# Kernel tuning notes

Hardware: AMD Instinct MI355X
Metric: run time of the kernel (lower is better)

Reference implementation:

```python
import jax, jax.numpy as jnp
import numpy as np

B, R, NM, H, P1, G1, RC1, LAT = 16384, 360, 200, 256, 512, 256, 256, 128


def _linear_params(k, out_f, in_f):
    s = 1.0 / np.sqrt(in_f)
    kw, kb = jax.random.split(k)
    W = jax.random.uniform(kw, (out_f, in_f), minval=-s, maxval=s, dtype=jnp.float32)
    b = jax.random.uniform(kb, (out_f,), minval=-s, maxval=s, dtype=jnp.float32)
    return W, b


def setup_inputs() -> dict:
    key = jax.random.key(0)
    ks = jax.random.split(key, 14)
    x_window = jax.random.normal(ks[0], (B, 3, R), dtype=jnp.float32)
    modes = jax.random.normal(ks[1], (R, NM), dtype=jnp.float32)
    mode_coeff = jax.random.normal(ks[2], (B, NM), dtype=jnp.float32)
    W1, b1 = _linear_params(ks[3], H, 3 * R)      # surrogate layer 1
    W2, b2 = _linear_params(ks[4], H, H)          # surrogate layer 2
    W3, b3 = _linear_params(ks[5], R, H)          # surrogate layer 3
    Wp1, bp1 = _linear_params(ks[6], P1, R * R)   # npi_proj
    Wp2, bp2 = _linear_params(ks[7], LAT, P1)
    Wg1, bg1 = _linear_params(ks[8], G1, NM)      # geo_proj
    Wg2, bg2 = _linear_params(ks[9], LAT, G1)
    Wr1, br1 = _linear_params(ks[10], RC1, LAT)   # recon
    Wr2, br2 = _linear_params(ks[11], R, RC1)
    return dict(x_window=x_window, modes=modes, mode_coeff=mode_coeff,
                W1=W1, b1=b1, W2=W2, b2=b2, W3=W3, b3=b3,
                Wp1=Wp1, bp1=bp1, Wp2=Wp2, bp2=bp2,
                Wg1=Wg1, bg1=bg1, Wg2=Wg2, bg2=bg2,
                Wr1=Wr1, br1=br1, Wr2=Wr2, br2=br2)


def reference(x_window, modes, mode_coeff,
              W1, b1, W2, b2, W3, b3,
              Wp1, bp1, Wp2, bp2,
              Wg1, bg1, Wg2, bg2,
              Wr1, br1, Wr2, br2):
    Bs = x_window.shape[0]
    Rr = W3.shape[0]
    # ---- NPI surrogate forward (needed for ReLU masks) ----
    z = x_window.reshape(Bs, 3 * Rr)                       # (B, 3R)
    h1 = z @ W1.T + b1                                     # (B, H)
    m1 = (h1 > 0).astype(z.dtype)
    h2 = (h1 * m1) @ W2.T + b2                             # (B, H)
    m2 = (h2 > 0).astype(z.dtype)
    # ---- EC: exact batch-mean Jacobian of the ReLU MLP w.r.t last timestep ----
    # mean_b [ W3 diag(m2_b) W2 diag(m1_b) W1_last ] = W3 @ (W2 * (m2^T m1 / B)) @ W1[:, -R:]
    G = (m2.T @ m1) / Bs                                   # (H, H)
    ec = W3 @ ((W2 * G) @ W1[:, -Rr:])                     # (R, R); row j = dy_j/dx
    ec = jax.lax.stop_gradient(ec)                         # create_graph=False in original
    # ---- projections ----
    ec_flat = ec.reshape(1, Rr * Rr)
    z_npi1 = jax.nn.relu(ec_flat @ Wp1.T + bp1) @ Wp2.T + bp2   # (1, LAT)
    z_npi = jnp.tile(z_npi1, (Bs, 1))                           # (B, LAT)
    z_geo = jax.nn.relu(mode_coeff @ Wg1.T + bg1) @ Wg2.T + bg2  # (B, LAT)
    zsum = z_npi + z_geo
    zn = zsum / jnp.maximum(jnp.linalg.norm(zsum, axis=-1, keepdims=True), 1e-12)
    recon = jax.nn.relu(zn @ Wr1.T + br1) @ Wr2.T + br2          # (B, R)
    return (z_npi, z_geo, zn, ec, recon)
```

## Files before the change

### kernel.cpp

```cpp
#include <hip/hip_runtime.h>

typedef __bf16 bf16x8 __attribute__((ext_vector_type(8)));
typedef __bf16 bf16x4 __attribute__((ext_vector_type(4)));
typedef float  f32x4  __attribute__((ext_vector_type(4)));

__device__ __forceinline__ f32x4 mfma_bf16(bf16x8 a, bf16x8 b, f32x4 c) {
  return __builtin_amdgcn_mfma_f32_16x16x32_bf16(a, b, c, 0, 0, 0);
}
__device__ __forceinline__ bf16x8 ldB(const __bf16* Bp, int kt, int NT, int nt,
                                      int lane) {
  return *reinterpret_cast<const bf16x8*>(Bp + (((size_t)kt * NT + nt) * 64 + lane) * 8);
}

__global__ void pack_all(const float* __restrict__ W1, const float* __restrict__ W2,
                         const float* __restrict__ Wg1, const float* __restrict__ Wg2,
                         const float* __restrict__ Wr1, const float* __restrict__ Wr2,
                         __bf16* __restrict__ W1p, __bf16* __restrict__ W2p,
                         __bf16* __restrict__ Wg1p, __bf16* __restrict__ Wg2p,
                         __bf16* __restrict__ Wr1p, __bf16* __restrict__ Wr2p,
                         float* __restrict__ G) {
  int bx = blockIdx.x;
  int lane = threadIdx.x;
  if (bx >= 1104) {
    float4* g = (float4*)G;
    int base = (bx - 1104) * 512 + lane;
#pragma unroll
    for (int i = 0; i < 8; ++i) g[base + i * 64] = make_float4(0.f, 0.f, 0.f, 0.f);
    return;
  }
  const float* W; __bf16* out; int N, K, NT, local;
  if (bx < 544)      { W = W1;  out = W1p;  N = 256; K = 1080; NT = 16; local = bx; }
  else if (bx < 672) { W = W2;  out = W2p;  N = 256; K = 256;  NT = 16; local = bx - 544; }
  else if (bx < 784) { W = Wg1; out = Wg1p; N = 256; K = 200;  NT = 16; local = bx - 672; }
  else if (bx < 848) { W = Wg2; out = Wg2p; N = 128; K = 256;  NT = 8;  local = bx - 784; }
  else if (bx < 912) { W = Wr1; out = Wr1p; N = 256; K = 128;  NT = 16; local = bx - 848; }
  else               { W = Wr2; out = Wr2p; N = 360; K = 256;  NT = 24; local = bx - 912; }
  int nt = local % NT, kt = local / NT;
  int n = nt * 16 + (lane & 15);
  int k0 = kt * 32 + (lane >> 4) * 8;
  bf16x8 v;
#pragma unroll
  for (int e = 0; e < 8; ++e) {
    int k = k0 + e;
    float xv = (n < N && k < K) ? W[(size_t)n * K + k] : 0.f;
    v[e] = (__bf16)xv;
  }
  *reinterpret_cast<bf16x8*>(out + ((size_t)local * 64 + lane) * 8) = v;
}

__global__ __launch_bounds__(256) void h1h2_fused(
    const float* __restrict__ x, const __bf16* __restrict__ W1p,
    const float* __restrict__ b1, const __bf16* __restrict__ W2p,
    const float* __restrict__ b2, __bf16* __restrict__ m1T,
    __bf16* __restrict__ m2T) {
  __shared__ __bf16 Alds[32][68];
  __shared__ __bf16 h1s[32][264];
  int tid = threadIdx.x;
  int lane = tid & 63, wid = tid >> 6;
  int rowBase = blockIdx.x * 32;
  int sr = tid >> 3, sc = (tid & 7) * 8;
  const float* aSrc = x + (size_t)(rowBase + sr) * 1080;
  f32x4 acc[2][4] = {};
  float4 c0a, c0b, c1a, c1b;
  auto LD = [&](int s, float4& a, float4& b) {
    int gk = s * 64 + sc;
    if (gk < 1080) {
      a = *(const float4*)(aSrc + gk);
      b = *(const float4*)(aSrc + gk + 4);
    } else {
      a = make_float4(0.f, 0.f, 0.f, 0.f);
      b = a;
    }
  };
  LD(0, c0a, c0b);
  LD(1, c1a, c1b);
  for (int s = 0; s < 17; ++s) {
    bf16x8 w8;
    w8[0] = (__bf16)c0a.x; w8[1] = (__bf16)c0a.y; w8[2] = (__bf16)c0a.z; w8[3] = (__bf16)c0a.w;
    w8[4] = (__bf16)c0b.x; w8[5] = (__bf16)c0b.y; w8[6] = (__bf16)c0b.z; w8[7] = (__bf16)c0b.w;
    *reinterpret_cast<bf16x8*>(&Alds[sr][sc]) = w8;
    __syncthreads();
    c0a = c1a; c0b = c1b;
    if (s + 2 < 17) LD(s + 2, c1a, c1b);
    int arow = lane & 15;
#pragma unroll
    for (int ks = 0; ks < 2; ++ks) {
      int ak = ks * 32 + (lane >> 4) * 8;
      bf16x8 a0 = *reinterpret_cast<const bf16x8*>(&Alds[arow][ak]);
      bf16x8 a1 = *reinterpret_cast<const bf16x8*>(&Alds[arow + 16][ak]);
      int kt = s * 2 + ks;
#pragma unroll
      for (int n = 0; n < 4; ++n) {
        bf16x8 bv = ldB(W1p, kt, 16, wid * 4 + n, lane);
        acc[0][n] = mfma_bf16(a0, bv, acc[0][n]);
        acc[1][n] = mfma_bf16(a1, bv, acc[1][n]);
      }
    }
    __syncthreads();
  }
  int q4 = (lane >> 4) * 4;
#pragma unroll
  for (int m = 0; m < 2; ++m)
#pragma unroll
    for (int n = 0; n < 4; ++n) {
      int col = wid * 64 + n * 16 + (lane & 15);
      float bb = b1[col];
#pragma unroll
      for (int j = 0; j < 4; ++j) {
        int rl = m * 16 + q4 + j;
        float h = acc[m][n][j] + bb;
        m1T[(size_t)col * 16384 + rowBase + rl] = (__bf16)(h > 0.f ? 1.f : 0.f);
        h1s[rl][col] = (__bf16)fmaxf(h, 0.f);
      }
    }
  __syncthreads();
  f32x4 acc2[2][4] = {};
#pragma unroll
  for (int ks = 0; ks < 8; ++ks) {
    int arow = lane & 15, ak = ks * 32 + (lane >> 4) * 8;
    bf16x8 a0 = *reinterpret_cast<const bf16x8*>(&h1s[arow][ak]);
    bf16x8 a1 = *reinterpret_cast<const bf16x8*>(&h1s[arow + 16][ak]);
#pragma unroll
    for (int n = 0; n < 4; ++n) {
      bf16x8 bv = ldB(W2p, ks, 16, wid * 4 + n, lane);
      acc2[0][n] = mfma_bf16(a0, bv, acc2[0][n]);
      acc2[1][n] = mfma_bf16(a1, bv, acc2[1][n]);
    }
  }
#pragma unroll
  for (int m = 0; m < 2; ++m)
#pragma unroll
    for (int n = 0; n < 4; ++n) {
      int col = wid * 64 + n * 16 + (lane & 15);
      float bb = b2[col];
#pragma unroll
      for (int j = 0; j < 4; ++j) {
        int rl = m * 16 + q4 + j;
        float h = acc2[m][n][j] + bb;
        m2T[(size_t)col * 16384 + rowBase + rl] = (__bf16)(h > 0.f ? 1.f : 0.f);
      }
    }
}

__global__ __launch_bounds__(256) void gemm_masks(
    const __bf16* __restrict__ m2T, const __bf16* __restrict__ m1T,
    float* __restrict__ G) {
  int tid = threadIdx.x;
  int lane = tid & 63, wid = tid >> 6;
  int wr = wid >> 1, wc = wid & 1;
  int ibase = blockIdx.x * 64, jbase = blockIdx.y * 64;
  size_t b0 = (size_t)blockIdx.z * 1024 + (lane >> 4) * 8;
  const __bf16* pa0 = m2T + (size_t)(ibase + wr * 32 + (lane & 15)) * 16384 + b0;
  const __bf16* pa1 = pa0 + (size_t)16 * 16384;
  const __bf16* pb0 = m1T + (size_t)(jbase + wc * 32 + (lane & 15)) * 16384 + b0;
  const __bf16* pb1 = pb0 + (size_t)16 * 16384;
  f32x4 acc[2][2] = {};
#pragma unroll 4
  for (int c = 0; c < 32; ++c) {
    bf16x8 a0 = *reinterpret_cast<const bf16x8*>(pa0 + c * 32);
    bf16x8 a1 = *reinterpret_cast<const bf16x8*>(pa1 + c * 32);
    bf16x8 bv0 = *reinterpret_cast<const bf16x8*>(pb0 + c * 32);
    bf16x8 bv1 = *reinterpret_cast<const bf16x8*>(pb1 + c * 32);
    acc[0][0] = mfma_bf16(a0, bv0, acc[0][0]);
    acc[0][1] = mfma_bf16(a0, bv1, acc[0][1]);
    acc[1][0] = mfma_bf16(a1, bv0, acc[1][0]);
    acc[1][1] = mfma_bf16(a1, bv1, acc[1][1]);
  }
  int q4 = (lane >> 4) * 4;
#pragma unroll
  for (int m = 0; m < 2; ++m)
#pragma unroll
    for (int n = 0; n < 2; ++n)
#pragma unroll
      for (int j = 0; j < 4; ++j) {
        int gi = ibase + wr * 32 + m * 16 + q4 + j;
        int gj = jbase + wc * 32 + n * 16 + (lane & 15);
        atomicAdd(&G[(size_t)gi * 256 + gj], acc[m][n][j] * (1.f / 16384.f));
      }
}

__global__ __launch_bounds__(256) void small_gemm(
    const float* __restrict__ A, const float* __restrict__ A2, int lda,
    const float* __restrict__ Bm, int ldb, float* __restrict__ C, int ldc,
    int M, int N, int K) {
  __shared__ float As[64][17];
  __shared__ float Bs[16][65];
  int t = threadIdx.x;
  int tx = t & 15, ty = t >> 4;
  int m0 = blockIdx.y * 64, n0 = blockIdx.x * 64;
  float acc[4][4] = {};
  for (int k0 = 0; k0 < K; k0 += 16) {
#pragma unroll
    for (int i = 0; i < 4; ++i) {
      int idx = t * 4 + i;
      int r = idx >> 4, kk = idx & 15;
      int gm = m0 + r, gk = k0 + kk;
      float v = (gm < M && gk < K) ? A[(size_t)gm * lda + gk] : 0.f;
      if (A2 && gm < M && gk < K) v *= A2[(size_t)gm * lda + gk];
      As[r][kk] = v;
      int kk2 = idx >> 6, cc = idx & 63;
      int gk2 = k0 + kk2, gn = n0 + cc;
      Bs[kk2][cc] = (gk2 < K && gn < N) ? Bm[(size_t)gk2 * ldb + gn] : 0.f;
    }
    __syncthreads();
#pragma unroll
    for (int kk = 0; kk < 16; ++kk)
#pragma unroll
      for (int i = 0; i < 4; ++i)
#pragma unroll
        for (int j = 0; j < 4; ++j)
          acc[i][j] += As[ty * 4 + i][kk] * Bs[kk][tx * 4 + j];
    __syncthreads();
  }
#pragma unroll
  for (int i = 0; i < 4; ++i)
#pragma unroll
    for (int j = 0; j < 4; ++j) {
      int gm = m0 + ty * 4 + i, gn = n0 + tx * 4 + j;
      if (gm < M && gn < N) C[(size_t)gm * ldc + gn] = acc[i][j];
    }
}

__global__ __launch_bounds__(512) void p_and_g1(
    const float* __restrict__ Wp1, const float* __restrict__ ec,
    const float* __restrict__ bp1, float* __restrict__ p,
    const float* __restrict__ mc, const __bf16* __restrict__ Wg1p,
    const float* __restrict__ bg1, const __bf16* __restrict__ Wg2p,
    const float* __restrict__ bg2, float* __restrict__ o_zgeo) {
  __shared__ __bf16 Alds[64][40];
  __shared__ __bf16 g1S[64][264];
  __shared__ float redw[8];
  int t = threadIdx.x;
  if (blockIdx.x < 512) {
    int row = blockIdx.x;
    const float4* w = (const float4*)(Wp1 + (size_t)row * 129600);
    const float4* e = (const float4*)ec;
    float s = 0.f;
    for (int i = t; i < 32400; i += 512) {
      float4 a = w[i], b = e[i];
      s += a.x * b.x + a.y * b.y + a.z * b.z + a.w * b.w;
    }
    for (int o = 32; o; o >>= 1) s += __shfl_down(s, o);
    if ((t & 63) == 0) redw[t >> 6] = s;
    __syncthreads();
    if (t == 0) {
      float tot = 0.f;
#pragma unroll
      for (int i = 0; i < 8; ++i) tot += redw[i];
      p[row] = fmaxf(tot + bp1[row], 0.f);
    }
  } else {
    int lane = t & 63, wid = t >> 6;
    int wr = wid >> 2, wc = wid & 3;
    int rowBase = (blockIdx.x - 512) * 64;
    int sr = t >> 3, sc = (t & 7) * 4;
    const float* aSrc = mc + (size_t)(rowBase + sr) * 200;
    int q4 = (lane >> 4) * 4;
    f32x4 acc[2][4] = {};
    for (int kt = 0; kt < 7; ++kt) {
      int gk = kt * 32 + sc;
      bf16x4 w4;
      if (gk < 200) {
        float4 v = *(const float4*)(aSrc + gk);
        w4[0] = (__bf16)v.x; w4[1] = (__bf16)v.y;
        w4[2] = (__bf16)v.z; w4[3] = (__bf16)v.w;
      } else {
        w4[0] = w4[1] = w4[2] = w4[3] = (__bf16)0.f;
      }
      *reinterpret_cast<bf16x4*>(&Alds[sr][sc]) = w4;
      __syncthreads();
      int arow = wr * 32 + (lane & 15), ak = (lane >> 4) * 8;
      bf16x8 a0 = *reinterpret_cast<const bf16x8*>(&Alds[arow][ak]);
      bf16x8 a1 = *reinterpret_cast<const bf16x8*>(&Alds[arow + 16][ak]);
#pragma unroll
      for (int n = 0; n < 4; ++n) {
        bf16x8 bv = ldB(Wg1p, kt, 16, wc * 4 + n, lane);
        acc[0][n] = mfma_bf16(a0, bv, acc[0][n]);
        acc[1][n] = mfma_bf16(a1, bv, acc[1][n]);
      }
      __syncthreads();
    }
#pragma unroll
    for (int m = 0; m < 2; ++m)
#pragma unroll
      for (int n = 0; n < 4; ++n) {
        int col = wc * 64 + n * 16 + (lane & 15);
        float bb = bg1[col];
#pragma unroll
        for (int j = 0; j < 4; ++j) {
          int rl = wr * 32 + m * 16 + q4 + j;
          g1S[rl][col] = (__bf16)fmaxf(acc[m][n][j] + bb, 0.f);
        }
      }
    __syncthreads();
    f32x4 acc2[2][2] = {};
#pragma unroll
    for (int ks = 0; ks < 8; ++ks) {
      int arow = wr * 32 + (lane & 15), ak = ks * 32 + (lane >> 4) * 8;
      bf16x8 a0 = *reinterpret_cast<const bf16x8*>(&g1S[arow][ak]);
      bf16x8 a1 = *reinterpret_cast<const bf16x8*>(&g1S[arow + 16][ak]);
#pragma unroll
      for (int n = 0; n < 2; ++n) {
        bf16x8 bv = ldB(Wg2p, ks, 8, wc * 2 + n, lane);
        acc2[0][n] = mfma_bf16(a0, bv, acc2[0][n]);
        acc2[1][n] = mfma_bf16(a1, bv, acc2[1][n]);
      }
    }
#pragma unroll
    for (int m = 0; m < 2; ++m)
#pragma unroll
      for (int n = 0; n < 2; ++n) {
        int col = wc * 32 + n * 16 + (lane & 15);
        float bb = bg2[col];
#pragma unroll
        for (int j = 0; j < 4; ++j) {
          int row = rowBase + wr * 32 + m * 16 + q4 + j;
          o_zgeo[(size_t)row * 128 + col] = acc2[m][n][j] + bb;
        }
      }
  }
}

__global__ void gemv_z(const float* __restrict__ p, const float* __restrict__ Wp2,
                       const float* __restrict__ bp2, float* __restrict__ znpi1) {
  int j = blockIdx.x;
  int t = threadIdx.x;
  const float4* w = (const float4*)(Wp2 + (size_t)j * 512);
  const float4* pp = (const float4*)p;
  float4 a0 = w[t], b0 = pp[t];
  float4 a1 = w[t + 64], b1 = pp[t + 64];
  float s = a0.x * b0.x + a0.y * b0.y + a0.z * b0.z + a0.w * b0.w +
            a1.x * b1.x + a1.y * b1.y + a1.z * b1.z + a1.w * b1.w;
  for (int o = 32; o; o >>= 1) s += __shfl_down(s, o);
  if (t == 0) znpi1[j] = s + bp2[j];
}

__global__ __launch_bounds__(512) void mega_tail(
    const float* __restrict__ zgeo, const float* __restrict__ znpi1,
    const __bf16* __restrict__ Wr1p, const float* __restrict__ br1,
    const __bf16* __restrict__ Wr2p, const float* __restrict__ br2,
    float* __restrict__ o_znpi, float* __restrict__ o_zn,
    float* __restrict__ o_rec) {
  __shared__ __bf16 r1S[64][264];
  __shared__ __bf16 znS[64][136];
  __shared__ float znpiS[128];
  int tid = threadIdx.x;
  int lane = tid & 63, wid = tid >> 6;
  int wr = wid >> 2, wc = wid & 3;
  int rowBase = blockIdx.x * 64;
  int q4 = (lane >> 4) * 4;
  if (tid < 128) znpiS[tid] = znpi1[tid];
  __syncthreads();
  {
    int rg = tid >> 5;
    int c4 = (tid & 31) * 4;
    float4 zp = make_float4(znpiS[c4], znpiS[c4 + 1], znpiS[c4 + 2], znpiS[c4 + 3]);
#pragma unroll
    for (int ri = 0; ri < 4; ++ri) {
      int rl = rg + ri * 16;
      int row = rowBase + rl;
      float4 zg = *(const float4*)(zgeo + (size_t)row * 128 + c4);
      float4 zs = make_float4(zg.x + zp.x, zg.y + zp.y, zg.z + zp.z, zg.w + zp.w);
      *(float4*)(o_znpi + (size_t)row * 128 + c4) = zp;
      float ss = zs.x * zs.x + zs.y * zs.y + zs.z * zs.z + zs.w * zs.w;
      ss += __shfl_xor(ss, 1);
      ss += __shfl_xor(ss, 2);
      ss += __shfl_xor(ss, 4);
      ss += __shfl_xor(ss, 8);
      ss += __shfl_xor(ss, 16);
      float rn = 1.f / fmaxf(sqrtf(ss), 1e-12f);
      float4 zn = make_float4(zs.x * rn, zs.y * rn, zs.z * rn, zs.w * rn);
      *(float4*)(o_zn + (size_t)row * 128 + c4) = zn;
      bf16x4 znb;
      znb[0] = (__bf16)zn.x; znb[1] = (__bf16)zn.y;
      znb[2] = (__bf16)zn.z; znb[3] = (__bf16)zn.w;
      *reinterpret_cast<bf16x4*>(&znS[rl][c4]) = znb;
    }
  }
  __syncthreads();
  {
    f32x4 acc[2][4] = {};
#pragma unroll
    for (int ks = 0; ks < 4; ++ks) {
      int arow = wr * 32 + (lane & 15), ak = ks * 32 + (lane >> 4) * 8;
      bf16x8 a0 = *reinterpret_cast<const bf16x8*>(&znS[arow][ak]);
      bf16x8 a1 = *reinterpret_cast<const bf16x8*>(&znS[arow + 16][ak]);
#pragma unroll
      for (int n = 0; n < 4; ++n) {
        bf16x8 bv = ldB(Wr1p, ks, 16, wc * 4 + n, lane);
        acc[0][n] = mfma_bf16(a0, bv, acc[0][n]);
        acc[1][n] = mfma_bf16(a1, bv, acc[1][n]);
      }
    }
#pragma unroll
    for (int m = 0; m < 2; ++m)
#pragma unroll
      for (int n = 0; n < 4; ++n) {
        int col = wc * 64 + n * 16 + (lane & 15);
        float bb = br1[col];
#pragma unroll
        for (int j = 0; j < 4; ++j) {
          int rl = wr * 32 + m * 16 + q4 + j;
          r1S[rl][col] = (__bf16)fmaxf(acc[m][n][j] + bb, 0.f);
        }
      }
  }
  __syncthreads();
  {
    f32x4 acc[2][6] = {};
#pragma unroll
    for (int ks = 0; ks < 8; ++ks) {
      int arow = wr * 32 + (lane & 15), ak = ks * 32 + (lane >> 4) * 8;
      bf16x8 a0 = *reinterpret_cast<const bf16x8*>(&r1S[arow][ak]);
      bf16x8 a1 = *reinterpret_cast<const bf16x8*>(&r1S[arow + 16][ak]);
#pragma unroll
      for (int n = 0; n < 6; ++n) {
        bf16x8 bv = ldB(Wr2p, ks, 24, wc * 6 + n, lane);
        acc[0][n] = mfma_bf16(a0, bv, acc[0][n]);
        acc[1][n] = mfma_bf16(a1, bv, acc[1][n]);
      }
    }
#pragma unroll
    for (int m = 0; m < 2; ++m)
#pragma unroll
      for (int n = 0; n < 6; ++n) {
        int col = wc * 96 + n * 16 + (lane & 15);
        if (col < 360) {
          float bb = br2[col];
#pragma unroll
          for (int j = 0; j < 4; ++j) {
            int rl = wr * 32 + m * 16 + q4 + j;
            o_rec[(size_t)(rowBase + rl) * 360 + col] = acc[m][n][j] + bb;
          }
        }
      }
  }
}

extern "C" void kernel_launch(void* const* d_in, const int* in_sizes, int n_in,
                              void* d_out, int out_size, void* d_ws,
                              size_t ws_size, hipStream_t stream) {
  (void)in_sizes; (void)n_in; (void)out_size; (void)ws_size;
  const float* x   = (const float*)d_in[0];
  const float* mc  = (const float*)d_in[2];
  const float* W1  = (const float*)d_in[3];  const float* b1  = (const float*)d_in[4];
  const float* W2  = (const float*)d_in[5];  const float* b2  = (const float*)d_in[6];
  const float* W3  = (const float*)d_in[7];
  const float* Wp1 = (const float*)d_in[9];  const float* bp1 = (const float*)d_in[10];
  const float* Wp2 = (const float*)d_in[11]; const float* bp2 = (const float*)d_in[12];
  const float* Wg1 = (const float*)d_in[13]; const float* bg1 = (const float*)d_in[14];
  const float* Wg2 = (const float*)d_in[15]; const float* bg2 = (const float*)d_in[16];
  const float* Wr1 = (const float*)d_in[17]; const float* br1 = (const float*)d_in[18];
  const float* Wr2 = (const float*)d_in[19]; const float* br2 = (const float*)d_in[20];

  float* out = (float*)d_out;
  float* o_znpi = out;
  float* o_zgeo = out + 2097152;
  float* o_zn   = out + 4194304;
  float* o_ec   = out + 6291456;
  float* o_rec  = out + 6421056;

  char* ws = (char*)d_ws;
  __bf16* m1T   = (__bf16*)(ws + 0);
  __bf16* m2T   = (__bf16*)(ws + 8388608);
  float*  G     = (float*)(ws + 16777216);
  float*  T     = (float*)(ws + 17039360);
  float*  p512  = (float*)(ws + 17432576);
  float*  znpi1 = (float*)(ws + 17434624);
  __bf16* W1p   = (__bf16*)(ws + 17435648);
  __bf16* W2p   = W1p  + (size_t)544 * 512;
  __bf16* Wg1p  = W2p  + (size_t)128 * 512;
  __bf16* Wg2p  = Wg1p + (size_t)112 * 512;
  __bf16* Wr1p  = Wg2p + (size_t)64 * 512;
  __bf16* Wr2p  = Wr1p + (size_t)64 * 512;

  pack_all<<<1136, 64, 0, stream>>>(W1, W2, Wg1, Wg2, Wr1, Wr2,
                                    W1p, W2p, Wg1p, Wg2p, Wr1p, Wr2p, G);
  h1h2_fused<<<512, 256, 0, stream>>>(x, W1p, b1, W2p, b2, m1T, m2T);
  gemm_masks<<<dim3(4, 4, 16), 256, 0, stream>>>(m2T, m1T, G);
  small_gemm<<<dim3(6, 4), 256, 0, stream>>>(W2, G, 256, W1 + 720, 1080, T, 384,
                                             256, 360, 256);
  small_gemm<<<dim3(6, 6), 256, 0, stream>>>(W3, nullptr, 256, T, 384, o_ec, 360,
                                             360, 360, 256);
  p_and_g1<<<768, 512, 0, stream>>>(Wp1, o_ec, bp1, p512, mc, Wg1p, bg1,
                                    Wg2p, bg2, o_zgeo);
  gemv_z<<<128, 64, 0, stream>>>(p512, Wp2, bp2, znpi1);
  mega_tail<<<256, 512, 0, stream>>>(o_zgeo, znpi1, Wr1p, br1, Wr2p, br2,
                                     o_znpi, o_zn, o_rec);
}
```

Measured before the change: 245.9 us.

## Merge pipeline into two persistent kernels synchronized by software grid barriers

Replaces the eight separate launches (pack, h1/h2, mask gemm, two small gemms, projection, gemv, tail) with two persistent 512-block kernels that use atomic-counter grid barriers between phases. Work is redistributed per block: 32-row tiles with 8 waves, the mask gemm split-K is changed to 32 chunks with wider tiles, and the z_npi gemv is folded into the tail. This is meant to remove launch overhead and inter-kernel gaps. In exchange it relies on all 512 blocks being co-resident for the spin barriers, adds a memset, and idles blocks during the small gemm phases.

```diff
diff --git a/kernel.cpp b/kernel.cpp
--- a/kernel.cpp
+++ b/kernel.cpp
@@ -12,250 +12,229 @@
   return *reinterpret_cast<const bf16x8*>(Bp + (((size_t)kt * NT + nt) * 64 + lane) * 8);
 }
 
-__global__ void pack_all(const float* __restrict__ W1, const float* __restrict__ W2,
-                         const float* __restrict__ Wg1, const float* __restrict__ Wg2,
-                         const float* __restrict__ Wr1, const float* __restrict__ Wr2,
-                         __bf16* __restrict__ W1p, __bf16* __restrict__ W2p,
-                         __bf16* __restrict__ Wg1p, __bf16* __restrict__ Wg2p,
-                         __bf16* __restrict__ Wr1p, __bf16* __restrict__ Wr2p,
-                         float* __restrict__ G) {
-  int bx = blockIdx.x;
-  int lane = threadIdx.x;
-  if (bx >= 1104) {
-    float4* g = (float4*)G;
-    int base = (bx - 1104) * 512 + lane;
-#pragma unroll
-    for (int i = 0; i < 8; ++i) g[base + i * 64] = make_float4(0.f, 0.f, 0.f, 0.f);
-    return;
-  }
-  const float* W; __bf16* out; int N, K, NT, local;
-  if (bx < 544)      { W = W1;  out = W1p;  N = 256; K = 1080; NT = 16; local = bx; }
-  else if (bx < 672) { W = W2;  out = W2p;  N = 256; K = 256;  NT = 16; local = bx - 544; }
-  else if (bx < 784) { W = Wg1; out = Wg1p; N = 256; K = 200;  NT = 16; local = bx - 672; }
-  else if (bx < 848) { W = Wg2; out = Wg2p; N = 128; K = 256;  NT = 8;  local = bx - 784; }
-  else if (bx < 912) { W = Wr1; out = Wr1p; N = 256; K = 128;  NT = 16; local = bx - 848; }
-  else               { W = Wr2; out = Wr2p; N = 360; K = 256;  NT = 24; local = bx - 912; }
-  int nt = local % NT, kt = local / NT;
-  int n = nt * 16 + (lane & 15);
-  int k0 = kt * 32 + (lane >> 4) * 8;
-  bf16x8 v;
-#pragma unroll
-  for (int e = 0; e < 8; ++e) {
-    int k = k0 + e;
-    float xv = (n < N && k < K) ? W[(size_t)n * K + k] : 0.f;
-    v[e] = (__bf16)xv;
-  }
-  *reinterpret_cast<bf16x8*>(out + ((size_t)local * 64 + lane) * 8) = v;
-}
-
-__global__ __launch_bounds__(256) void h1h2_fused(
-    const float* __restrict__ x, const __bf16* __restrict__ W1p,
-    const float* __restrict__ b1, const __bf16* __restrict__ W2p,
-    const float* __restrict__ b2, __bf16* __restrict__ m1T,
-    __bf16* __restrict__ m2T) {
-  __shared__ __bf16 Alds[32][68];
-  __shared__ __bf16 h1s[32][264];
-  int tid = threadIdx.x;
+__device__ __forceinline__ void gridbar(int* cnt, int target) {
+  __syncthreads();
+  if (threadIdx.x == 0) {
+    __threadfence();
+    __hip_atomic_fetch_add(cnt, 1, __ATOMIC_RELEASE, __HIP_MEMORY_SCOPE_AGENT);
+    while (__hip_atomic_load(cnt, __ATOMIC_RELAXED, __HIP_MEMORY_SCOPE_AGENT) < target)
+      __builtin_amdgcn_s_sleep(4);
+    __threadfence();
+  }
+  __syncthreads();
+}
+
+__device__ void small_body(char* SM, int t,
+                           const float* __restrict__ A, const float* __restrict__ A2,
+                           int lda, const float* __restrict__ Bm, int ldb,
+                           float* __restrict__ C, int ldc,
+                           int M, int N, int K, int m0, int n0) {
+  float (*As)[17] = (float(*)[17])SM;
+  float (*Bs)[65] = (float(*)[65])(SM + 4352);
+  bool act = t < 256;
+  int tx = t & 15, ty = (t >> 4) & 15;
+  float acc[4][4] = {};
+  for (int k0 = 0; k0 < K; k0 += 16) {
+    if (act) {
+#pragma unroll
+      for (int i = 0; i < 4; ++i) {
+        int idx = t * 4 + i;
+        int r = idx >> 4, kk = idx & 15;
+        int gm = m0 + r, gk = k0 + kk;
+        float v = (gm < M && gk < K) ? A[(size_t)gm * lda + gk] : 0.f;
+        if (A2 && gm < M && gk < K) v *= A2[(size_t)gm * lda + gk];
+        As[r][kk] = v;
+        int kk2 = idx >> 6, cc = idx & 63;
+        int gk2 = k0 + kk2, gn = n0 + cc;
+        Bs[kk2][cc] = (gk2 < K && gn < N) ? Bm[(size_t)gk2 * ldb + gn] : 0.f;
+      }
+    }
+    __syncthreads();
+    if (act) {
+#pragma unroll
+      for (int kk = 0; kk < 16; ++kk)
+#pragma unroll
+        for (int i = 0; i < 4; ++i)
+#pragma unroll
+          for (int j = 0; j < 4; ++j)
+            acc[i][j] += As[ty * 4 + i][kk] * Bs[kk][tx * 4 + j];
+    }
+    __syncthreads();
+  }
+  if (act) {
+#pragma unroll
+    for (int i = 0; i < 4; ++i)
+#pragma unroll
+      for (int j = 0; j < 4; ++j) {
+        int gm = m0 + ty * 4 + i, gn = n0 + tx * 4 + j;
+        if (gm < M && gn < N) C[(size_t)gm * ldc + gn] = acc[i][j];
+      }
+  }
+}
+
+__global__ __launch_bounds__(512, 4) void mega1(
+    const float* __restrict__ x,
+    const float* __restrict__ W1, const float* __restrict__ b1,
+    const float* __restrict__ W2, const float* __restrict__ b2,
+    const float* __restrict__ W3, const float* __restrict__ mc,
+    const float* __restrict__ Wg1, const float* __restrict__ bg1,
+    const float* __restrict__ Wg2, const float* __restrict__ bg2,
+    const float* __restrict__ Wr1, const float* __restrict__ Wr2,
+    __bf16* __restrict__ W1p, __bf16* __restrict__ W2p,
+    __bf16* __restrict__ Wg1p, __bf16* __restrict__ Wg2p,
+    __bf16* __restrict__ Wr1p, __bf16* __restrict__ Wr2p,
+    __bf16* __restrict__ m1T, __bf16* __restrict__ m2T,
+    float* __restrict__ G, float* __restrict__ T,
+    float* __restrict__ o_zgeo, float* __restrict__ o_ec,
+    int* __restrict__ cnt) {
+  __shared__ __align__(16) char SM[38912];
+  int tid = threadIdx.x, bid = blockIdx.x;
   int lane = tid & 63, wid = tid >> 6;
-  int rowBase = blockIdx.x * 32;
-  int sr = tid >> 3, sc = (tid & 7) * 8;
-  const float* aSrc = x + (size_t)(rowBase + sr) * 1080;
-  f32x4 acc[2][4] = {};
-  float4 c0a, c0b, c1a, c1b;
-  auto LD = [&](int s, float4& a, float4& b) {
-    int gk = s * 64 + sc;
-    if (gk < 1080) {
-      a = *(const float4*)(aSrc + gk);
-      b = *(const float4*)(aSrc + gk + 4);
-    } else {
-      a = make_float4(0.f, 0.f, 0.f, 0.f);
-      b = a;
-    }
-  };
-  LD(0, c0a, c0b);
-  LD(1, c1a, c1b);
-  for (int s = 0; s < 17; ++s) {
-    bf16x8 w8;
-    w8[0] = (__bf16)c0a.x; w8[1] = (__bf16)c0a.y; w8[2] = (__bf16)c0a.z; w8[3] = (__bf16)c0a.w;
-    w8[4] = (__bf16)c0b.x; w8[5] = (__bf16)c0b.y; w8[6] = (__bf16)c0b.z; w8[7] = (__bf16)c0b.w;
-    *reinterpret_cast<bf16x8*>(&Alds[sr][sc]) = w8;
-    __syncthreads();
-    c0a = c1a; c0b = c1b;
-    if (s + 2 < 17) LD(s + 2, c1a, c1b);
-    int arow = lane & 15;
-#pragma unroll
-    for (int ks = 0; ks < 2; ++ks) {
-      int ak = ks * 32 + (lane >> 4) * 8;
-      bf16x8 a0 = *reinterpret_cast<const bf16x8*>(&Alds[arow][ak]);
-      bf16x8 a1 = *reinterpret_cast<const bf16x8*>(&Alds[arow + 16][ak]);
-      int kt = s * 2 + ks;
-#pragma unroll
-      for (int n = 0; n < 4; ++n) {
-        bf16x8 bv = ldB(W1p, kt, 16, wid * 4 + n, lane);
-        acc[0][n] = mfma_bf16(a0, bv, acc[0][n]);
-        acc[1][n] = mfma_bf16(a1, bv, acc[1][n]);
-      }
-    }
-    __syncthreads();
-  }
   int q4 = (lane >> 4) * 4;
-#pragma unroll
-  for (int m = 0; m < 2; ++m)
+
+  {
+    int gid = bid * 8 + wid;
+    if (gid < 1104) {
+      const float* W; __bf16* outp; int N, K, NT, local;
+      if (gid < 544)      { W = W1;  outp = W1p;  N = 256; K = 1080; NT = 16; local = gid; }
+      else if (gid < 672) { W = W2;  outp = W2p;  N = 256; K = 256;  NT = 16; local = gid - 544; }
+      else if (gid < 784) { W = Wg1; outp = Wg1p; N = 256; K = 200;  NT = 16; local = gid - 672; }
+      else if (gid < 848) { W = Wg2; outp = Wg2p; N = 128; K = 256;  NT = 8;  local = gid - 784; }
+      else if (gid < 912) { W = Wr1; outp = Wr1p; N = 256; K = 128;  NT = 16; local = gid - 848; }
+      else                { W = Wr2; outp = Wr2p; N = 360; K = 256;  NT = 24; local = gid - 912; }
+      int nt = local % NT, kt = local / NT;
+      int n = nt * 16 + (lane & 15);
+      int k0 = kt * 32 + (lane >> 4) * 8;
+      bf16x8 v;
+#pragma unroll
+      for (int e = 0; e < 8; ++e) {
+        int k = k0 + e;
+        float xv = (n < N && k < K) ? W[(size_t)n * K + k] : 0.f;
+        v[e] = (__bf16)xv;
+      }
+      *reinterpret_cast<bf16x8*>(outp + ((size_t)local * 64 + lane) * 8) = v;
+    } else if (gid < 1136) {
+      float4* g = (float4*)G;
+      int base = (gid - 1104) * 512 + lane;
+#pragma unroll
+      for (int i = 0; i < 8; ++i) g[base + i * 64] = make_float4(0.f, 0.f, 0.f, 0.f);
+    }
+  }
+  gridbar(cnt, 512);
+
+  {
+    __bf16 (*Alds)[68] = (__bf16(*)[68])SM;
+    __bf16 (*h1s)[264] = (__bf16(*)[264])(SM + 4352);
+    int wr16 = (wid >> 2) * 16, wc4 = (wid & 3) * 4, wc64 = (wid & 3) * 64;
+    int rowBase = bid * 32;
+    int sr = tid >> 4, sc = (tid & 15) * 4;
+    const float* aSrc = x + (size_t)(rowBase + sr) * 1080;
+    f32x4 acc[4] = {};
+    float4 c0, c1;
+    auto LD = [&](int s, float4& d) {
+      int gk = s * 64 + sc;
+      d = (gk < 1080) ? *(const float4*)(aSrc + gk) : make_float4(0.f, 0.f, 0.f, 0.f);
+    };
+    LD(0, c0);
+    LD(1, c1);
+    for (int s = 0; s < 17; ++s) {
+      bf16x4 w4;
+      w4[0] = (__bf16)c0.x; w4[1] = (__bf16)c0.y;
+      w4[2] = (__bf16)c0.z; w4[3] = (__bf16)c0.w;
+      *reinterpret_cast<bf16x4*>(&Alds[sr][sc]) = w4;
+      __syncthreads();
+      c0 = c1;
+      if (s + 2 < 17) LD(s + 2, c1);
+      int arow = wr16 + (lane & 15);
+#pragma unroll
+      for (int ks = 0; ks < 2; ++ks) {
+        int ak = ks * 32 + (lane >> 4) * 8;
+        bf16x8 a0 = *reinterpret_cast<const bf16x8*>(&Alds[arow][ak]);
+        int kt = s * 2 + ks;
+#pragma unroll
+        for (int n = 0; n < 4; ++n) {
+          bf16x8 bv = ldB(W1p, kt, 16, wc4 + n, lane);
+          acc[n] = mfma_bf16(a0, bv, acc[n]);
+        }
+      }
+      __syncthreads();
+    }
 #pragma unroll
     for (int n = 0; n < 4; ++n) {
-      int col = wid * 64 + n * 16 + (lane & 15);
+      int col = wc64 + n * 16 + (lane & 15);
       float bb = b1[col];
 #pragma unroll
       for (int j = 0; j < 4; ++j) {
-        int rl = m * 16 + q4 + j;
-        float h = acc[m][n][j] + bb;
+        int rl = wr16 + q4 + j;
+        float h = acc[n][j] + bb;
         m1T[(size_t)col * 16384 + rowBase + rl] = (__bf16)(h > 0.f ? 1.f : 0.f);
         h1s[rl][col] = (__bf16)fmaxf(h, 0.f);
       }
     }
-  __syncthreads();
-  f32x4 acc2[2][4] = {};
-#pragma unroll
-  for (int ks = 0; ks < 8; ++ks) {
-    int arow = lane & 15, ak = ks * 32 + (lane >> 4) * 8;
-    bf16x8 a0 = *reinterpret_cast<const bf16x8*>(&h1s[arow][ak]);
-    bf16x8 a1 = *reinterpret_cast<const bf16x8*>(&h1s[arow + 16][ak]);
+    __syncthreads();
+    f32x4 acc2[4] = {};
+#pragma unroll
+    for (int ks = 0; ks < 8; ++ks) {
+      int arow = wr16 + (lane & 15), ak = ks * 32 + (lane >> 4) * 8;
+      bf16x8 a0 = *reinterpret_cast<const bf16x8*>(&h1s[arow][ak]);
+#pragma unroll
+      for (int n = 0; n < 4; ++n) {
+        bf16x8 bv = ldB(W2p, ks, 16, wc4 + n, lane);
+        acc2[n] = mfma_bf16(a0, bv, acc2[n]);
+      }
+    }
 #pragma unroll
     for (int n = 0; n < 4; ++n) {
-      bf16x8 bv = ldB(W2p, ks, 16, wid * 4 + n, lane);
-      acc2[0][n] = mfma_bf16(a0, bv, acc2[0][n]);
-      acc2[1][n] = mfma_bf16(a1, bv, acc2[1][n]);
-    }
-  }
-#pragma unroll
-  for (int m = 0; m < 2; ++m)
-#pragma unroll
-    for (int n = 0; n < 4; ++n) {
-      int col = wid * 64 + n * 16 + (lane & 15);
+      int col = wc64 + n * 16 + (lane & 15);
       float bb = b2[col];
 #pragma unroll
       for (int j = 0; j < 4; ++j) {
-        int rl = m * 16 + q4 + j;
-        float h = acc2[m][n][j] + bb;
+        int rl = wr16 + q4 + j;
+        float h = acc2[n][j] + bb;
         m2T[(size_t)col * 16384 + rowBase + rl] = (__bf16)(h > 0.f ? 1.f : 0.f);
       }
     }
-}
-
-__global__ __launch_bounds__(256) void gemm_masks(
-    const __bf16* __restrict__ m2T, const __bf16* __restrict__ m1T,
-    float* __restrict__ G) {
-  int tid = threadIdx.x;
-  int lane = tid & 63, wid = tid >> 6;
-  int wr = wid >> 1, wc = wid & 1;
-  int ibase = blockIdx.x * 64, jbase = blockIdx.y * 64;
-  size_t b0 = (size_t)blockIdx.z * 1024 + (lane >> 4) * 8;
-  const __bf16* pa0 = m2T + (size_t)(ibase + wr * 32 + (lane & 15)) * 16384 + b0;
-  const __bf16* pa1 = pa0 + (size_t)16 * 16384;
-  const __bf16* pb0 = m1T + (size_t)(jbase + wc * 32 + (lane & 15)) * 16384 + b0;
-  const __bf16* pb1 = pb0 + (size_t)16 * 16384;
-  f32x4 acc[2][2] = {};
+  }
+  gridbar(cnt, 1024);
+
+  if (bid < 256) {
+    int iz = bid & 31, ij = bid >> 5;
+    int ibase = (ij >> 1) * 64, jbase = (ij & 1) * 128;
+    int wr = wid >> 2, wc = wid & 3;
+    size_t b0 = (size_t)iz * 512 + (lane >> 4) * 8;
+    const __bf16* pa0 = m2T + (size_t)(ibase + wr * 32 + (lane & 15)) * 16384 + b0;
+    const __bf16* pa1 = pa0 + (size_t)16 * 16384;
+    const __bf16* pb0 = m1T + (size_t)(jbase + wc * 32 + (lane & 15)) * 16384 + b0;
+    const __bf16* pb1 = pb0 + (size_t)16 * 16384;
+    f32x4 acc[2][2] = {};
 #pragma unroll 4
-  for (int c = 0; c < 32; ++c) {
-    bf16x8 a0 = *reinterpret_cast<const bf16x8*>(pa0 + c * 32);
-    bf16x8 a1 = *reinterpret_cast<const bf16x8*>(pa1 + c * 32);
-    bf16x8 bv0 = *reinterpret_cast<const bf16x8*>(pb0 + c * 32);
-    bf16x8 bv1 = *reinterpret_cast<const bf16x8*>(pb1 + c * 32);
-    acc[0][0] = mfma_bf16(a0, bv0, acc[0][0]);
-    acc[0][1] = mfma_bf16(a0, bv1, acc[0][1]);
-    acc[1][0] = mfma_bf16(a1, bv0, acc[1][0]);
-    acc[1][1] = mfma_bf16(a1, bv1, acc[1][1]);
-  }
-  int q4 = (lane >> 4) * 4;
-#pragma unroll
-  for (int m = 0; m < 2; ++m)
-#pragma unroll
-    for (int n = 0; n < 2; ++n)
-#pragma unroll
-      for (int j = 0; j < 4; ++j) {
-        int gi = ibase + wr * 32 + m * 16 + q4 + j;
-        int gj = jbase + wc * 32 + n * 16 + (lane & 15);
-        atomicAdd(&G[(size_t)gi * 256 + gj], acc[m][n][j] * (1.f / 16384.f));
-      }
-}
-
-__global__ __launch_bounds__(256) void small_gemm(
-    const float* __restrict__ A, const float* __restrict__ A2, int lda,
-    const float* __restrict__ Bm, int ldb, float* __restrict__ C, int ldc,
-    int M, int N, int K) {
-  __shared__ float As[64][17];
-  __shared__ float Bs[16][65];
-  int t = threadIdx.x;
-  int tx = t & 15, ty = t >> 4;
-  int m0 = blockIdx.y * 64, n0 = blockIdx.x * 64;
-  float acc[4][4] = {};
-  for (int k0 = 0; k0 < K; k0 += 16) {
-#pragma unroll
-    for (int i = 0; i < 4; ++i) {
-      int idx = t * 4 + i;
-      int r = idx >> 4, kk = idx & 15;
-      int gm = m0 + r, gk = k0 + kk;
-      float v = (gm < M && gk < K) ? A[(size_t)gm * lda + gk] : 0.f;
-      if (A2 && gm < M && gk < K) v *= A2[(size_t)gm * lda + gk];
-      As[r][kk] = v;
-      int kk2 = idx >> 6, cc = idx & 63;
-      int gk2 = k0 + kk2, gn = n0 + cc;
-      Bs[kk2][cc] = (gk2 < K && gn < N) ? Bm[(size_t)gk2 * ldb + gn] : 0.f;
-    }
-    __syncthreads();
-#pragma unroll
-    for (int kk = 0; kk < 16; ++kk)
-#pragma unroll
-      for (int i = 0; i < 4; ++i)
-#pragma unroll
-        for (int j = 0; j < 4; ++j)
-          acc[i][j] += As[ty * 4 + i][kk] * Bs[kk][tx * 4 + j];
-    __syncthreads();
-  }
-#pragma unroll
-  for (int i = 0; i < 4; ++i)
-#pragma unroll
-    for (int j = 0; j < 4; ++j) {
-      int gm = m0 + ty * 4 + i, gn = n0 + tx * 4 + j;
-      if (gm < M && gn < N) C[(size_t)gm * ldc + gn] = acc[i][j];
-    }
-}
-
-__global__ __launch_bounds__(512) void p_and_g1(
-    const float* __restrict__ Wp1, const float* __restrict__ ec,
-    const float* __restrict__ bp1, float* __restrict__ p,
-    const float* __restrict__ mc, const __bf16* __restrict__ Wg1p,
-    const float* __restrict__ bg1, const __bf16* __restrict__ Wg2p,
-    const float* __restrict__ bg2, float* __restrict__ o_zgeo) {
-  __shared__ __bf16 Alds[64][40];
-  __shared__ __bf16 g1S[64][264];
-  __shared__ float redw[8];
-  int t = threadIdx.x;
-  if (blockIdx.x < 512) {
-    int row = blockIdx.x;
-    const float4* w = (const float4*)(Wp1 + (size_t)row * 129600);
-    const float4* e = (const float4*)ec;
-    float s = 0.f;
-    for (int i = t; i < 32400; i += 512) {
-      float4 a = w[i], b = e[i];
-      s += a.x * b.x + a.y * b.y + a.z * b.z + a.w * b.w;
-    }
-    for (int o = 32; o; o >>= 1) s += __shfl_down(s, o);
-    if ((t & 63) == 0) redw[t >> 6] = s;
-    __syncthreads();
-    if (t == 0) {
-      float tot = 0.f;
-#pragma unroll
-      for (int i = 0; i < 8; ++i) tot += redw[i];
-      p[row] = fmaxf(tot + bp1[row], 0.f);
-    }
+    for (int c = 0; c < 16; ++c) {
+      bf16x8 a0 = *reinterpret_cast<const bf16x8*>(pa0 + c * 32);
+      bf16x8 a1 = *reinterpret_cast<const bf16x8*>(pa1 + c * 32);
+      bf16x8 bv0 = *reinterpret_cast<const bf16x8*>(pb0 + c * 32);
+      bf16x8 bv1 = *reinterpret_cast<const bf16x8*>(pb1 + c * 32);
+      acc[0][0] = mfma_bf16(a0, bv0, acc[0][0]);
+      acc[0][1] = mfma_bf16(a0, bv1, acc[0][1]);
+      acc[1][0] = mfma_bf16(a1, bv0, acc[1][0]);
+      acc[1][1] = mfma_bf16(a1, bv1, acc[1][1]);
+    }
+#pragma unroll
+    for (int m = 0; m < 2; ++m)
+#pragma unroll
+      for (int n = 0; n < 2; ++n)
+#pragma unroll
+        for (int j = 0; j < 4; ++j) {
+          int gi = ibase + wr * 32 + m * 16 + q4 + j;
+          int gj = jbase + wc * 32 + n * 16 + (lane & 15);
+          atomicAdd(&G[(size_t)gi * 256 + gj], acc[m][n][j] * (1.f / 16384.f));
+        }
   } else {
-    int lane = t & 63, wid = t >> 6;
+    __bf16 (*Alds2)[40] = (__bf16(*)[40])SM;
+    __bf16 (*g1S)[264] = (__bf16(*)[264])(SM + 5120);
     int wr = wid >> 2, wc = wid & 3;
-    int rowBase = (blockIdx.x - 512) * 64;
-    int sr = t >> 3, sc = (t & 7) * 4;
+    int rowBase = (bid - 256) * 64;
+    int sr = tid >> 3, sc = (tid & 7) * 4;
     const float* aSrc = mc + (size_t)(rowBase + sr) * 200;
-    int q4 = (lane >> 4) * 4;
     f32x4 acc[2][4] = {};
     for (int kt = 0; kt < 7; ++kt) {
       int gk = kt * 32 + sc;
@@ -267,11 +246,11 @@
       } else {
         w4[0] = w4[1] = w4[2] = w4[3] = (__bf16)0.f;
       }
-      *reinterpret_cast<bf16x4*>(&Alds[sr][sc]) = w4;
+      *reinterpret_cast<bf16x4*>(&Alds2[sr][sc]) = w4;
       __syncthreads();
       int arow = wr * 32 + (lane & 15), ak = (lane >> 4) * 8;
-      bf16x8 a0 = *reinterpret_cast<const bf16x8*>(&Alds[arow][ak]);
-      bf16x8 a1 = *reinterpret_cast<const bf16x8*>(&Alds[arow + 16][ak]);
+      bf16x8 a0 = *reinterpret_cast<const bf16x8*>(&Alds2[arow][ak]);
+      bf16x8 a1 = *reinterpret_cast<const bf16x8*>(&Alds2[arow + 16][ak]);
 #pragma unroll
       for (int n = 0; n < 4; ++n) {
         bf16x8 bv = ldB(Wg1p, kt, 16, wc * 4 + n, lane);
@@ -319,109 +298,137 @@
         }
       }
   }
-}
-
-__global__ void gemv_z(const float* __restrict__ p, const float* __restrict__ Wp2,
-                       const float* __restrict__ bp2, float* __restrict__ znpi1) {
-  int j = blockIdx.x;
-  int t = threadIdx.x;
-  const float4* w = (const float4*)(Wp2 + (size_t)j * 512);
-  const float4* pp = (const float4*)p;
-  float4 a0 = w[t], b0 = pp[t];
-  float4 a1 = w[t + 64], b1 = pp[t + 64];
-  float s = a0.x * b0.x + a0.y * b0.y + a0.z * b0.z + a0.w * b0.w +
-            a1.x * b1.x + a1.y * b1.y + a1.z * b1.z + a1.w * b1.w;
-  for (int o = 32; o; o >>= 1) s += __shfl_down(s, o);
-  if (t == 0) znpi1[j] = s + bp2[j];
-}
-
-__global__ __launch_bounds__(512) void mega_tail(
-    const float* __restrict__ zgeo, const float* __restrict__ znpi1,
+  gridbar(cnt, 1536);
+
+  if (bid < 24)
+    small_body(SM, tid, W2, G, 256, W1 + 720, 1080, T, 384,
+               256, 360, 256, (bid / 6) * 64, (bid % 6) * 64);
+  gridbar(cnt, 2048);
+
+  if (bid < 36)
+    small_body(SM, tid, W3, nullptr, 256, T, 384, o_ec, 360,
+               360, 360, 256, (bid / 6) * 64, (bid % 6) * 64);
+}
+
+__global__ __launch_bounds__(512, 4) void mega2(
+    const float* __restrict__ Wp1, const float* __restrict__ ec,
+    const float* __restrict__ bp1, float* __restrict__ p,
+    const float* __restrict__ Wp2, const float* __restrict__ bp2,
+    const float* __restrict__ zgeo,
     const __bf16* __restrict__ Wr1p, const float* __restrict__ br1,
     const __bf16* __restrict__ Wr2p, const float* __restrict__ br2,
     float* __restrict__ o_znpi, float* __restrict__ o_zn,
-    float* __restrict__ o_rec) {
-  __shared__ __bf16 r1S[64][264];
-  __shared__ __bf16 znS[64][136];
-  __shared__ float znpiS[128];
-  int tid = threadIdx.x;
+    float* __restrict__ o_rec, int* __restrict__ cnt) {
+  __shared__ __align__(16) char SM[28160];
+  int tid = threadIdx.x, bid = blockIdx.x;
   int lane = tid & 63, wid = tid >> 6;
-  int wr = wid >> 2, wc = wid & 3;
-  int rowBase = blockIdx.x * 64;
   int q4 = (lane >> 4) * 4;
-  if (tid < 128) znpiS[tid] = znpi1[tid];
-  __syncthreads();
+
   {
-    int rg = tid >> 5;
-    int c4 = (tid & 31) * 4;
-    float4 zp = make_float4(znpiS[c4], znpiS[c4 + 1], znpiS[c4 + 2], znpiS[c4 + 3]);
-#pragma unroll
-    for (int ri = 0; ri < 4; ++ri) {
-      int rl = rg + ri * 16;
-      int row = rowBase + rl;
-      float4 zg = *(const float4*)(zgeo + (size_t)row * 128 + c4);
-      float4 zs = make_float4(zg.x + zp.x, zg.y + zp.y, zg.z + zp.z, zg.w + zp.w);
-      *(float4*)(o_znpi + (size_t)row * 128 + c4) = zp;
-      float ss = zs.x * zs.x + zs.y * zs.y + zs.z * zs.z + zs.w * zs.w;
-      ss += __shfl_xor(ss, 1);
-      ss += __shfl_xor(ss, 2);
-      ss += __shfl_xor(ss, 4);
-      ss += __shfl_xor(ss, 8);
-      ss += __shfl_xor(ss, 16);
-      float rn = 1.f / fmaxf(sqrtf(ss), 1e-12f);
-      float4 zn = make_float4(zs.x * rn, zs.y * rn, zs.z * rn, zs.w * rn);
-      *(float4*)(o_zn + (size_t)row * 128 + c4) = zn;
-      bf16x4 znb;
-      znb[0] = (__bf16)zn.x; znb[1] = (__bf16)zn.y;
-      znb[2] = (__bf16)zn.z; znb[3] = (__bf16)zn.w;
-      *reinterpret_cast<bf16x4*>(&znS[rl][c4]) = znb;
-    }
-  }
-  __syncthreads();
+    float* redw = (float*)SM;
+    const float4* w = (const float4*)(Wp1 + (size_t)bid * 129600);
+    const float4* e = (const float4*)ec;
+    float s = 0.f;
+    for (int i = tid; i < 32400; i += 512) {
+      float4 a = w[i], b = e[i];
+      s += a.x * b.x + a.y * b.y + a.z * b.z + a.w * b.w;
+    }
+    for (int o = 32; o; o >>= 1) s += __shfl_down(s, o);
+    if (lane == 0) redw[wid] = s;
+    __syncthreads();
+    if (tid == 0) {
+      float tot = 0.f;
+#pragma unroll
+      for (int i = 0; i < 8; ++i) tot += redw[i];
+      p[bid] = fmaxf(tot + bp1[bid], 0.f);
+    }
+  }
+  gridbar(cnt, 512);
+
   {
-    f32x4 acc[2][4] = {};
-#pragma unroll
-    for (int ks = 0; ks < 4; ++ks) {
-      int arow = wr * 32 + (lane & 15), ak = ks * 32 + (lane >> 4) * 8;
-      bf16x8 a0 = *reinterpret_cast<const bf16x8*>(&znS[arow][ak]);
-      bf16x8 a1 = *reinterpret_cast<const bf16x8*>(&znS[arow + 16][ak]);
-#pragma unroll
-      for (int n = 0; n < 4; ++n) {
-        bf16x8 bv = ldB(Wr1p, ks, 16, wc * 4 + n, lane);
-        acc[0][n] = mfma_bf16(a0, bv, acc[0][n]);
-        acc[1][n] = mfma_bf16(a1, bv, acc[1][n]);
-      }
-    }
-#pragma unroll
-    for (int m = 0; m < 2; ++m)
+    float* pS = (float*)SM;
+    float* znpiS = (float*)(SM + 2048);
+    __bf16 (*znS)[136] = (__bf16(*)[136])(SM + 2560);
+    __bf16 (*r1S)[264] = (__bf16(*)[264])(SM + 11264);
+    int rowBase = bid * 32;
+    pS[tid] = p[tid];
+    __syncthreads();
+    {
+      int col = tid >> 2, q = tid & 3;
+      const float4* w = (const float4*)(Wp2 + (size_t)col * 512 + q * 128);
+      const float4* pv = (const float4*)(pS + q * 128);
+      float s = 0.f;
+#pragma unroll
+      for (int i = 0; i < 32; ++i) {
+        float4 a = w[i], b = pv[i];
+        s += a.x * b.x + a.y * b.y + a.z * b.z + a.w * b.w;
+      }
+      s += __shfl_xor(s, 1);
+      s += __shfl_xor(s, 2);
+      if (q == 0) znpiS[col] = s + bp2[col];
+    }
+    __syncthreads();
+    {
+      int rg = tid >> 5, c4 = (tid & 31) * 4;
+      float4 zp = make_float4(znpiS[c4], znpiS[c4 + 1], znpiS[c4 + 2], znpiS[c4 + 3]);
+#pragma unroll
+      for (int ri = 0; ri < 2; ++ri) {
+        int rl = rg + ri * 16;
+        int row = rowBase + rl;
+        float4 zg = *(const float4*)(zgeo + (size_t)row * 128 + c4);
+        float4 zs = make_float4(zg.x + zp.x, zg.y + zp.y, zg.z + zp.z, zg.w + zp.w);
+        *(float4*)(o_znpi + (size_t)row * 128 + c4) = zp;
+        float ss = zs.x * zs.x + zs.y * zs.y + zs.z * zs.z + zs.w * zs.w;
+        ss += __shfl_xor(ss, 1);
+        ss += __shfl_xor(ss, 2);
+        ss += __shfl_xor(ss, 4);
+        ss += __shfl_xor(ss, 8);
+        ss += __shfl_xor(ss, 16);
+        float rn = 1.f / fmaxf(sqrtf(ss), 1e-12f);
+        float4 zn = make_float4(zs.x * rn, zs.y * rn, zs.z * rn, zs.w * rn);
+        *(float4*)(o_zn + (size_t)row * 128 + c4) = zn;
+        bf16x4 znb;
+        znb[0] = (__bf16)zn.x; znb[1] = (__bf16)zn.y;
+        znb[2] = (__bf16)zn.z; znb[3] = (__bf16)zn.w;
+        *reinterpret_cast<bf16x4*>(&znS[rl][c4]) = znb;
+      }
+    }
+    __syncthreads();
+    int wr16 = (wid >> 2) * 16, wc = wid & 3;
+    {
+      f32x4 acc[4] = {};
+#pragma unroll
+      for (int ks = 0; ks < 4; ++ks) {
+        int arow = wr16 + (lane & 15), ak = ks * 32 + (lane >> 4) * 8;
+        bf16x8 a0 = *reinterpret_cast<const bf16x8*>(&znS[arow][ak]);
+#pragma unroll
+        for (int n = 0; n < 4; ++n) {
+          bf16x8 bv = ldB(Wr1p, ks, 16, wc * 4 + n, lane);
+          acc[n] = mfma_bf16(a0, bv, acc[n]);
+        }
+      }
 #pragma unroll
       for (int n = 0; n < 4; ++n) {
         int col = wc * 64 + n * 16 + (lane & 15);
         float bb = br1[col];
 #pragma unroll
-        for (int j = 0; j < 4; ++j) {
-          int rl = wr * 32 + m * 16 + q4 + j;
-          r1S[rl][col] = (__bf16)fmaxf(acc[m][n][j] + bb, 0.f);
-        }
-      }
-  }
-  __syncthreads();
-  {
-    f32x4 acc[2][6] = {};
-#pragma unroll
-    for (int ks = 0; ks < 8; ++ks) {
-      int arow = wr * 32 + (lane & 15), ak = ks * 32 + (lane >> 4) * 8;
-      bf16x8 a0 = *reinterpret_cast<const bf16x8*>(&r1S[arow][ak]);
-      bf16x8 a1 = *reinterpret_cast<const bf16x8*>(&r1S[arow + 16][ak]);
-#pragma unroll
-      for (int n = 0; n < 6; ++n) {
-        bf16x8 bv = ldB(Wr2p, ks, 24, wc * 6 + n, lane);
-        acc[0][n] = mfma_bf16(a0, bv, acc[0][n]);
-        acc[1][n] = mfma_bf16(a1, bv, acc[1][n]);
-      }
-    }
-#pragma unroll
-    for (int m = 0; m < 2; ++m)
+        for (int j = 0; j < 4; ++j)
+          r1S[wr16 + q4 + j][col] = (__bf16)fmaxf(acc[n][j] + bb, 0.f);
+      }
+    }
+    __syncthreads();
+    {
+      f32x4 acc[6] = {};
+#pragma unroll
+      for (int ks = 0; ks < 8; ++ks) {
+        int arow = wr16 + (lane & 15), ak = ks * 32 + (lane >> 4) * 8;
+        bf16x8 a0 = *reinterpret_cast<const bf16x8*>(&r1S[arow][ak]);
+#pragma unroll
+        for (int n = 0; n < 6; ++n) {
+          bf16x8 bv = ldB(Wr2p, ks, 24, wc * 6 + n, lane);
+          acc[n] = mfma_bf16(a0, bv, acc[n]);
+        }
+      }
 #pragma unroll
       for (int n = 0; n < 6; ++n) {
         int col = wc * 96 + n * 16 + (lane & 15);
@@ -429,11 +436,12 @@
           float bb = br2[col];
 #pragma unroll
           for (int j = 0; j < 4; ++j) {
-            int rl = wr * 32 + m * 16 + q4 + j;
-            o_rec[(size_t)(rowBase + rl) * 360 + col] = acc[m][n][j] + bb;
+            int rl = wr16 + q4 + j;
+            o_rec[(size_t)(rowBase + rl) * 360 + col] = acc[n][j] + bb;
           }
         }
       }
+    }
   }
 }
 
@@ -466,25 +474,19 @@
   float*  G     = (float*)(ws + 16777216);
   float*  T     = (float*)(ws + 17039360);
   float*  p512  = (float*)(ws + 17432576);
-  float*  znpi1 = (float*)(ws + 17434624);
-  __bf16* W1p   = (__bf16*)(ws + 17435648);
+  __bf16* W1p   = (__bf16*)(ws + 17434624);
   __bf16* W2p   = W1p  + (size_t)544 * 512;
   __bf16* Wg1p  = W2p  + (size_t)128 * 512;
   __bf16* Wg2p  = Wg1p + (size_t)112 * 512;
   __bf16* Wr1p  = Wg2p + (size_t)64 * 512;
   __bf16* Wr2p  = Wr1p + (size_t)64 * 512;
-
-  pack_all<<<1136, 64, 0, stream>>>(W1, W2, Wg1, Wg2, Wr1, Wr2,
-                                    W1p, W2p, Wg1p, Wg2p, Wr1p, Wr2p, G);
-  h1h2_fused<<<512, 256, 0, stream>>>(x, W1p, b1, W2p, b2, m1T, m2T);
-  gemm_masks<<<dim3(4, 4, 16), 256, 0, stream>>>(m2T, m1T, G);
-  small_gemm<<<dim3(6, 4), 256, 0, stream>>>(W2, G, 256, W1 + 720, 1080, T, 384,
-                                             256, 360, 256);
-  small_gemm<<<dim3(6, 6), 256, 0, stream>>>(W3, nullptr, 256, T, 384, o_ec, 360,
-                                             360, 360, 256);
-  p_and_g1<<<768, 512, 0, stream>>>(Wp1, o_ec, bp1, p512, mc, Wg1p, bg1,
-                                    Wg2p, bg2, o_zgeo);
-  gemv_z<<<128, 64, 0, stream>>>(p512, Wp2, bp2, znpi1);
-  mega_tail<<<256, 512, 0, stream>>>(o_zgeo, znpi1, Wr1p, br1, Wr2p, br2,
-                                     o_znpi, o_zn, o_rec);
-}
+  int*    cnt   = (int*)(ws + 18565120);
+
+  hipMemsetAsync(cnt, 0, 64, stream);
+  mega1<<<512, 512, 0, stream>>>(x, W1, b1, W2, b2, W3, mc, Wg1, bg1, Wg2, bg2,
+                                 Wr1, Wr2, W1p, W2p, Wg1p, Wg2p, Wr1p, Wr2p,
+                                 m1T, m2T, G, T, o_zgeo, o_ec, cnt);
+  mega2<<<512, 512, 0, stream>>>(Wp1, o_ec, bp1, p512, Wp2, bp2, o_zgeo,
+                                 Wr1p, br1, Wr2p, br2, o_znpi, o_zn, o_rec,
+                                 cnt + 1);
+}
```

New measurement: 546.8 us. +122.3%, slower.
